# Optimization experiments

Measured on AMD Instinct MI355X. Metric: run time of the kernel, lower is better.

The kernel has to match this reference:

```python
import jax, jax.numpy as jnp
import numpy as np
import math

N_EMBD = 1024
N_HEADS = 16
B, T = 4, 2048

def setup_inputs() -> dict:
    key = jax.random.key(0)
    k1, k2, k3 = jax.random.split(key, 3)
    x = jax.random.normal(k1, (B, T, N_EMBD), dtype=jnp.float32)
    scale = 1.0 / math.sqrt(N_EMBD)
    W_attn = jax.random.normal(k2, (N_EMBD, 3 * N_EMBD), dtype=jnp.float32) * scale
    W_proj = jax.random.normal(k3, (N_EMBD, N_EMBD), dtype=jnp.float32) * scale
    return {"x": x, "W_attn": W_attn, "W_proj": W_proj}

def reference(x, W_attn, W_proj):
    Bb, Tt, C = x.shape
    hd = C // N_HEADS
    qkv = x @ W_attn  # [B,T,3C]
    q, k, v = jnp.split(qkv, 3, axis=-1)
    # [B,H,T,hd]
    q = q.reshape(Bb, Tt, N_HEADS, hd).transpose(0, 2, 1, 3)
    k = k.reshape(Bb, Tt, N_HEADS, hd).transpose(0, 2, 1, 3)
    v = v.reshape(Bb, Tt, N_HEADS, hd).transpose(0, 2, 1, 3)
    att = jnp.einsum('bhqd,bhkd->bhqk', q, k) * (1.0 / math.sqrt(hd))
    mask = jnp.tril(jnp.ones((Tt, Tt), dtype=bool))
    att = jnp.where(mask[None, None], att, -jnp.inf)
    att = jax.nn.softmax(att, axis=-1)
    out = jnp.einsum('bhqk,bhkd->bhqd', att, v)
    out = out.transpose(0, 2, 1, 3).reshape(Bb, Tt, C)
    return out @ W_proj
```

## Files before the change

kernel.cpp:

```cpp
#include <hip/hip_runtime.h>
#include <cstddef>
#include <cstdint>

typedef __attribute__((ext_vector_type(8))) _Float16 half8;
typedef __attribute__((ext_vector_type(4))) _Float16 half4;
typedef __attribute__((ext_vector_type(4))) float f32x4;
typedef __attribute__((ext_vector_type(16))) float f32x16;

#define N_EMBD 1024
#define N_HEADS 16
#define BATCH 4
#define SEQ 2048
#define C3 3072
#define HD 64

__device__ inline uint32_t pk2(float x, float y) {
    auto h2 = __builtin_amdgcn_cvt_pkrtz(x, y);
    uint32_t u;
    __builtin_memcpy(&u, &h2, 4);
    return u;
}

__device__ inline void swap32(uint32_t& a, uint32_t& b) {
    asm volatile("v_permlane32_swap_b32 %0, %1" : "+v"(a), "+v"(b));
}

__device__ inline float exp2_hw(float x) {
    float r;
    asm("v_exp_f32 %0, %1" : "=v"(r) : "v"(x));
    return r;
}

__global__ void cvt_f32_f16(const float* __restrict__ in, _Float16* __restrict__ out, int n) {
    int i = (blockIdx.x * 256 + threadIdx.x) * 4;
    if (i >= n) return;
    float4 v = *(const float4*)(in + i);
    half4 h;
    h[0] = (_Float16)v.x; h[1] = (_Float16)v.y; h[2] = (_Float16)v.z; h[3] = (_Float16)v.w;
    *(half4*)(out + i) = h;
}

__global__ void transpose_cvt(const float* __restrict__ in, _Float16* __restrict__ out,
                              int R, int Ncols) {
    __shared__ float tile[32][33];
    int n0 = blockIdx.x * 32, r0 = blockIdx.y * 32;
    int tx = threadIdx.x, ty = threadIdx.y;
#pragma unroll
    for (int i = 0; i < 32; i += 8)
        tile[ty + i][tx] = in[(size_t)(r0 + ty + i) * Ncols + n0 + tx];
    __syncthreads();
#pragma unroll
    for (int i = 0; i < 32; i += 8)
        out[(size_t)(n0 + ty + i) * R + r0 + tx] = (_Float16)tile[tx][ty + i];
}

__global__ void transpose_v(const _Float16* __restrict__ qkv, _Float16* __restrict__ vT) {
    __shared__ _Float16 tile[32][36];
    int t0 = blockIdx.x * 32;
    int bhd = blockIdx.y;
    int bh = bhd >> 1, dh = bhd & 1;
    int b = bh >> 4, h = bh & 15;
    int tx = threadIdx.x, ty = threadIdx.y;
#pragma unroll
    for (int i = 0; i < 32; i += 8)
        tile[ty + i][tx] = qkv[(size_t)(b * SEQ + t0 + ty + i) * C3 + 2 * N_EMBD + h * HD + dh * 32 + tx];
    __syncthreads();
#pragma unroll
    for (int i = 0; i < 32; i += 8)
        vT[((size_t)bh * HD + dh * 32 + ty + i) * SEQ + t0 + tx] = tile[tx][ty + i];
}

__device__ inline void store1(float* p, float v) { *p = v; }
__device__ inline void store1(_Float16* p, float v) { *p = (_Float16)v; }

template <typename OutT>
__global__ __launch_bounds__(512, 1) void gemm192(
    const _Float16* __restrict__ A, const _Float16* __restrict__ Bt,
    OutT* __restrict__ C, int M, int N, int K) {
    __shared__ _Float16 Al[2][256 * 64];
    __shared__ _Float16 Bl[2][192 * 64];
    const int tid = threadIdx.x;
    const int lane = tid & 63, wave = tid >> 6;
    const int l15 = lane & 15, l4 = lane >> 4;
    const int wm = wave >> 2, wn = wave & 3;

    const int nwg = gridDim.x, nbx = N / 192;
    int wg = blockIdx.x;
    if ((nwg & 7) == 0) { int cpx = nwg >> 3; wg = (wg & 7) * cpx + (wg >> 3); }
    const int row0 = (wg / nbx) * 256, col0 = (wg % nbx) * 192;
    const int TAU = K >> 6;

    const int srow = tid >> 3, su = tid & 7;
    const int usrc8 = (su ^ (srow & 7)) * 8;
    auto stageAu = [&](int unit, int ts) {
        __builtin_amdgcn_global_load_lds(
            (const __attribute__((address_space(1))) void*)(A + (size_t)(row0 + unit * 64 + srow) * K + ts * 64 + usrc8),
            (__attribute__((address_space(3))) void*)(&Al[ts & 1][unit * 64 * 64 + tid * 8]), 16, 0, 0);
    };
    auto stageBu = [&](int unit, int ts) {
        __builtin_amdgcn_global_load_lds(
            (const __attribute__((address_space(1))) void*)(Bt + (size_t)(col0 + unit * 64 + srow) * K + ts * 64 + usrc8),
            (__attribute__((address_space(3))) void*)(&Bl[ts & 1][unit * 64 * 64 + tid * 8]), 16, 0, 0);
    };
    auto stageTile = [&](int ts) {
        stageAu(0, ts); stageAu(1, ts); stageAu(2, ts); stageAu(3, ts);
        stageBu(0, ts); stageBu(1, ts); stageBu(2, ts);
    };

    f32x4 acc[8][3] = {};
    stageTile(0); stageTile(1);
    asm volatile("s_waitcnt vmcnt(7)" ::: "memory");
    __builtin_amdgcn_s_barrier();

    half8 a[4][2], b[3][2];
    for (int tau = 0; tau < TAU; ++tau) {
        const _Float16* Ab = &Al[tau & 1][0];
        const _Float16* Bb = &Bl[tau & 1][0];
        const bool t2 = (tau + 2 < TAU);

#pragma unroll
        for (int m = 0; m < 4; ++m)
#pragma unroll
            for (int ks = 0; ks < 2; ++ks) {
                int r = wm * 128 + m * 16 + l15;
                a[m][ks] = *(const half8*)(Ab + r * 64 + (((ks * 4 + l4) ^ (r & 7)) * 8));
            }
#pragma unroll
        for (int n = 0; n < 3; ++n)
#pragma unroll
            for (int ks = 0; ks < 2; ++ks) {
                int r = wn * 48 + n * 16 + l15;
                b[n][ks] = *(const half8*)(Bb + r * 64 + (((ks * 4 + l4) ^ (r & 7)) * 8));
            }
        __builtin_amdgcn_s_barrier();
        __builtin_amdgcn_s_setprio(1);
#pragma unroll
        for (int m = 0; m < 4; ++m)
#pragma unroll
            for (int n = 0; n < 2; ++n)
#pragma unroll
                for (int ks = 0; ks < 2; ++ks)
                    acc[m][n] = __builtin_amdgcn_mfma_f32_16x16x32_f16(a[m][ks], b[n][ks], acc[m][n], 0, 0, 0);
        __builtin_amdgcn_s_setprio(0);
        __builtin_amdgcn_s_barrier();

        if (t2) { stageBu(0, tau + 2); stageBu(1, tau + 2); stageBu(2, tau + 2); }
        __builtin_amdgcn_s_barrier();
        __builtin_amdgcn_s_setprio(1);
#pragma unroll
        for (int m = 0; m < 4; ++m)
#pragma unroll
            for (int ks = 0; ks < 2; ++ks)
                acc[m][2] = __builtin_amdgcn_mfma_f32_16x16x32_f16(a[m][ks], b[2][ks], acc[m][2], 0, 0, 0);
        __builtin_amdgcn_s_setprio(0);
        __builtin_amdgcn_s_barrier();

#pragma unroll
        for (int m = 0; m < 4; ++m)
#pragma unroll
            for (int ks = 0; ks < 2; ++ks) {
                int r = wm * 128 + 64 + m * 16 + l15;
                a[m][ks] = *(const half8*)(Ab + r * 64 + (((ks * 4 + l4) ^ (r & 7)) * 8));
            }
        if (t2) { stageAu(0, tau + 2); stageAu(2, tau + 2); }
        __builtin_amdgcn_s_barrier();
        __builtin_amdgcn_s_setprio(1);
#pragma unroll
        for (int m = 0; m < 4; ++m)
#pragma unroll
            for (int n = 0; n < 2; ++n)
#pragma unroll
                for (int ks = 0; ks < 2; ++ks)
                    acc[4 + m][n] = __builtin_amdgcn_mfma_f32_16x16x32_f16(a[m][ks], b[n][ks], acc[4 + m][n], 0, 0, 0);
        __builtin_amdgcn_s_setprio(0);
        __builtin_amdgcn_s_barrier();

        if (t2) { stageAu(1, tau + 2); stageAu(3, tau + 2); }
        __builtin_amdgcn_s_barrier();
        __builtin_amdgcn_s_setprio(1);
#pragma unroll
        for (int m = 0; m < 4; ++m)
#pragma unroll
            for (int ks = 0; ks < 2; ++ks)
                acc[4 + m][2] = __builtin_amdgcn_mfma_f32_16x16x32_f16(a[m][ks], b[2][ks], acc[4 + m][2], 0, 0, 0);
        __builtin_amdgcn_s_setprio(0);
        if (tau <= TAU - 3) {
            asm volatile("s_waitcnt vmcnt(7)" ::: "memory");
        } else if (tau == TAU - 2) {
            asm volatile("s_waitcnt vmcnt(0)" ::: "memory");
        }
        __builtin_amdgcn_s_barrier();
    }

#pragma unroll
    for (int mi = 0; mi < 8; ++mi)
#pragma unroll
        for (int ni = 0; ni < 3; ++ni)
#pragma unroll
            for (int j = 0; j < 4; ++j) {
                int r = row0 + wm * 128 + (mi >> 2) * 64 + (mi & 3) * 16 + l4 * 4 + j;
                int c = col0 + wn * 48 + ni * 16 + l15;
                store1(C + (size_t)r * N + c, acc[mi][ni][j]);
            }
}

template <typename OutT>
__global__ __launch_bounds__(256, 2) void gemm_h(
    const _Float16* __restrict__ A, const _Float16* __restrict__ Bt,
    OutT* __restrict__ C, int M, int N, int K) {
    __shared__ _Float16 Al[128 * 32];
    __shared__ _Float16 Bl[128 * 32];
    const int tid = threadIdx.x;
    const int wave = tid >> 6, lane = tid & 63;
    const int l15 = lane & 15, l4 = lane >> 4;
    const int gx = gridDim.x;
    int lin = blockIdx.y * gx + blockIdx.x;
    int bcol, brow;
    if ((gx & 7) == 0) {
        int cpx = gx >> 3;
        int xcd = lin & 7;
        int idx = lin >> 3;
        bcol = xcd * cpx + idx % cpx;
        brow = idx / cpx;
    } else { bcol = blockIdx.x; brow = blockIdx.y; }
    const int row0 = brow * 128, col0 = bcol * 128;
    const int wm = wave >> 1, wn = wave & 1;
    f32x4 acc[4][4] = {};
    for (int k0 = 0; k0 < K; k0 += 32) {
#pragma unroll
        for (int i = 0; i < 2; ++i) {
            int c = tid + 256 * i;
            int r = c >> 2, c8 = (c & 3) * 8;
            __builtin_amdgcn_global_load_lds(
                (const __attribute__((address_space(1))) void*)(A + (size_t)(row0 + r) * K + k0 + c8),
                (__attribute__((address_space(3))) void*)(Al + (size_t)(wave * 64 + 256 * i) * 8),
                16, 0, 0);
        }
#pragma unroll
        for (int i = 0; i < 2; ++i) {
            int c = tid + 256 * i;
            int r = c >> 2, c8 = (c & 3) * 8;
            __builtin_amdgcn_global_load_lds(
                (const __attribute__((address_space(1))) void*)(Bt + (size_t)(col0 + r) * K + k0 + c8),
                (__attribute__((address_space(3))) void*)(Bl + (size_t)(wave * 64 + 256 * i) * 8),
                16, 0, 0);
        }
        __syncthreads();
        half8 a[4], b[4];
#pragma unroll
        for (int m = 0; m < 4; ++m)
            a[m] = *(const half8*)(Al + (wm * 64 + m * 16 + l15) * 32 + l4 * 8);
#pragma unroll
        for (int n = 0; n < 4; ++n)
            b[n] = *(const half8*)(Bl + (wn * 64 + n * 16 + l15) * 32 + l4 * 8);
        __builtin_amdgcn_s_setprio(1);
#pragma unroll
        for (int m = 0; m < 4; ++m)
#pragma unroll
            for (int n = 0; n < 4; ++n)
                acc[m][n] = __builtin_amdgcn_mfma_f32_16x16x32_f16(a[m], b[n], acc[m][n], 0, 0, 0);
        __builtin_amdgcn_s_setprio(0);
        __syncthreads();
    }
#pragma unroll
    for (int m = 0; m < 4; ++m)
#pragma unroll
        for (int n = 0; n < 4; ++n)
#pragma unroll
            for (int j = 0; j < 4; ++j) {
                int r = row0 + wm * 64 + m * 16 + l4 * 4 + j;
                int cc = col0 + wn * 64 + n * 16 + l15;
                store1(C + (size_t)r * N + cc, acc[m][n][j]);
            }
}

__global__ __launch_bounds__(512, 4) void attn_kernel(const _Float16* __restrict__ qkv,
                                                      const _Float16* __restrict__ vT,
                                                      _Float16* __restrict__ ao) {
    const int bid = blockIdx.x;
    const int qt8 = (bid < 256) ? (bid >> 6) : 7 - ((bid - 256) >> 6);
    const int bh = bid & 63;
    const int b = bh >> 4, h = bh & 15;
    const int tid = threadIdx.x, lane = tid & 63;
    const int wave = tid >> 6;
    const int l31 = lane & 31, L = lane >> 5;

    __shared__ _Float16 Kl[3][64 * 64];
    __shared__ _Float16 Vl[3][64 * 64];

    const float qscale = 0.125f * 1.44269504089f;
    const float NEGC = -4.0f * 1.44269504089f;

    const int q0w = qt8 * 256 + wave * 32;
    const int q_g = q0w + l31;
    const int nt = 4 * qt8 + 4;

    const int s_row = tid >> 3;
    const int s_u8 = ((tid & 7) ^ (s_row & 7)) * 8;
    auto stage = [&](int t, int buf) {
        __builtin_amdgcn_global_load_lds(
            (const __attribute__((address_space(1))) void*)(qkv + (size_t)(b * SEQ + t * 64 + s_row) * C3 + N_EMBD + h * HD + s_u8),
            (__attribute__((address_space(3))) void*)(&Kl[buf][tid * 8]), 16, 0, 0);
        __builtin_amdgcn_global_load_lds(
            (const __attribute__((address_space(1))) void*)(vT + ((size_t)bh * HD + s_row) * SEQ + t * 64 + s_u8),
            (__attribute__((address_space(3))) void*)(&Vl[buf][tid * 8]), 16, 0, 0);
    };

    stage(0, 0);
    stage(1, 1);

    half8 qb[4];
#pragma unroll
    for (int ks = 0; ks < 4; ++ks) {
        half8 v = *(const half8*)(qkv + (size_t)(b * SEQ + q_g) * C3 + h * HD + ks * 16 + L * 8);
#pragma unroll
        for (int e = 0; e < 8; ++e) v[e] = (_Float16)((float)v[e] * qscale);
        qb[ks] = v;
    }
    half8 onesf;
#pragma unroll
    for (int e = 0; e < 8; ++e) onesf[e] = (_Float16)1.0f;

    const f32x16 cinit = (f32x16)(NEGC);
    f32x16 o[2];
    o[0] = (f32x16)(0.f);
    o[1] = (f32x16)(0.f);
    f32x16 lac = (f32x16)(0.f);

    asm volatile("s_waitcnt vmcnt(6)" ::: "memory");
    __builtin_amdgcn_s_barrier();

    int cur = 0;
    for (int t = 0; t < nt; ++t) {
        const int kv0 = t * 64;
        int sb = cur + 2; if (sb >= 3) sb -= 3;
        if (t + 2 < nt) stage(t + 2, sb);

        if (kv0 <= q0w + 31) {
            const _Float16* Kb = &Kl[cur][0];
            const _Float16* Vb = &Vl[cur][0];
            f32x16 s[2];
            __builtin_amdgcn_s_setprio(1);
#pragma unroll
            for (int kb = 0; kb < 2; ++kb) {
                const int key = kb * 32 + l31;
                {
                    half8 kf = *(const half8*)(Kb + key * 64 + ((L ^ (key & 7)) * 8));
                    s[kb] = __builtin_amdgcn_mfma_f32_32x32x16_f16(kf, qb[0], cinit, 0, 0, 0);
                }
#pragma unroll
                for (int ks = 1; ks < 4; ++ks) {
                    half8 kf = *(const half8*)(Kb + key * 64 + (((ks * 2 + L) ^ (key & 7)) * 8));
                    s[kb] = __builtin_amdgcn_mfma_f32_32x32x16_f16(kf, qb[ks], s[kb], 0, 0, 0);
                }
            }
            __builtin_amdgcn_s_setprio(0);
            const bool needmask = (kv0 + 63 > q0w);
#pragma unroll
            for (int kb = 0; kb < 2; ++kb) {
#pragma unroll
                for (int r = 0; r < 16; ++r) {
                    float v = exp2_hw(s[kb][r]);
                    if (needmask) {
                        int key_g = kv0 + kb * 32 + (r & 3) + 8 * (r >> 2) + 4 * L;
                        v = (key_g > q_g) ? 0.f : v;
                    }
                    s[kb][r] = v;
                }
            }
            half8 paf[4];
#pragma unroll
            for (int kb = 0; kb < 2; ++kb)
#pragma unroll
                for (int hf = 0; hf < 2; ++hf) {
                    const int bse = hf * 8;
                    uint32_t a0 = pk2(s[kb][bse + 0], s[kb][bse + 1]);
                    uint32_t b0 = pk2(s[kb][bse + 4], s[kb][bse + 5]);
                    swap32(a0, b0);
                    uint32_t a1 = pk2(s[kb][bse + 2], s[kb][bse + 3]);
                    uint32_t b1 = pk2(s[kb][bse + 6], s[kb][bse + 7]);
                    swap32(a1, b1);
                    uint32_t w[4] = {a0, a1, b0, b1};
                    __builtin_memcpy(&paf[kb * 2 + hf], w, 16);
                }
            __builtin_amdgcn_s_setprio(1);
#pragma unroll
            for (int ks = 0; ks < 4; ++ks) {
                lac = __builtin_amdgcn_mfma_f32_32x32x16_f16(paf[ks], onesf, lac, 0, 0, 0);
#pragma unroll
                for (int db = 0; db < 2; ++db) {
                    const int d = db * 32 + l31;
                    half8 vb = *(const half8*)(Vb + d * 64 + (((ks * 2 + L) ^ (d & 7)) * 8));
                    o[db] = __builtin_amdgcn_mfma_f32_32x32x16_f16(paf[ks], vb, o[db], 0, 0, 0);
                }
            }
            __builtin_amdgcn_s_setprio(0);
        }

        if (t + 2 < nt) {
            asm volatile("s_waitcnt vmcnt(2)" ::: "memory");
        } else if (t + 1 < nt) {
            asm volatile("s_waitcnt vmcnt(0)" ::: "memory");
        }
        __builtin_amdgcn_s_barrier();
        ++cur; if (cur == 3) cur = 0;
    }

#pragma unroll
    for (int db = 0; db < 2; ++db)
#pragma unroll
        for (int r = 0; r < 16; ++r) {
            int qg = q0w + (r & 3) + 8 * (r >> 2) + 4 * L;
            ao[(size_t)(b * SEQ + qg) * N_EMBD + h * HD + db * 32 + l31] =
                (_Float16)(o[db][r] / lac[r]);
        }
}

extern "C" void kernel_launch(void* const* d_in, const int* in_sizes, int n_in,
                              void* d_out, int out_size, void* d_ws, size_t ws_size,
                              hipStream_t stream) {
    const float* x  = (const float*)d_in[0];
    const float* Wa = (const float*)d_in[1];
    const float* Wp = (const float*)d_in[2];
    float* out = (float*)d_out;

    const int M = BATCH * SEQ;
    _Float16* xh  = (_Float16*)d_ws;
    _Float16* WaT = xh + (size_t)M * N_EMBD;
    _Float16* WpT = WaT + (size_t)C3 * N_EMBD;
    _Float16* qkv = WpT + (size_t)N_EMBD * N_EMBD;
    _Float16* ao  = qkv + (size_t)M * C3;
    _Float16* vT  = xh;

    int nx = M * N_EMBD;
    cvt_f32_f16<<<nx / 4 / 256, 256, 0, stream>>>(x, xh, nx);
    dim3 tb(32, 8);
    transpose_cvt<<<dim3(C3 / 32, N_EMBD / 32), tb, 0, stream>>>(Wa, WaT, N_EMBD, C3);
    transpose_cvt<<<dim3(N_EMBD / 32, N_EMBD / 32), tb, 0, stream>>>(Wp, WpT, N_EMBD, N_EMBD);

    gemm192<_Float16><<<dim3((M / 256) * (C3 / 192)), 512, 0, stream>>>(xh, WaT, qkv, M, C3, N_EMBD);

    transpose_v<<<dim3(SEQ / 32, BATCH * N_HEADS * 2), tb, 0, stream>>>(qkv, vT);

    attn_kernel<<<dim3(512), 512, 0, stream>>>(qkv, vT, ao);

    gemm_h<float><<<dim3(N_EMBD / 128, M / 128), 256, 0, stream>>>(ao, WpT, out, M, N_EMBD, N_EMBD);
}
```

Measured before the change: 188.1 us.

## Split attention into 128-query tiles processed as causal-balanced pairs per block

Each attention block now has 4 waves (256 threads) instead of 8. It handles two 128-query tiles in sequence, tile pairp and its mirror 15-pairp, so every block does about the same amount of causal work. Previously each block handled one 256-query tile, and the launch order was arranged to balance the load. Staging now issues two loads per thread for K and V, and the wait counts are adjusted to match. Smaller tiles waste less work on the masked diagonal, but each K/V tile loaded into LDS is shared by fewer waves, and the pipeline is restarted between the two passes.

```diff
diff --git a/kernel.cpp b/kernel.cpp
--- a/kernel.cpp
+++ b/kernel.cpp
@@ -274,11 +274,11 @@
             }
 }
 
-__global__ __launch_bounds__(512, 4) void attn_kernel(const _Float16* __restrict__ qkv,
+__global__ __launch_bounds__(256, 3) void attn_kernel(const _Float16* __restrict__ qkv,
                                                       const _Float16* __restrict__ vT,
                                                       _Float16* __restrict__ ao) {
     const int bid = blockIdx.x;
-    const int qt8 = (bid < 256) ? (bid >> 6) : 7 - ((bid - 256) >> 6);
+    const int pairp = bid >> 6;
     const int bh = bid & 63;
     const int b = bh >> 4, h = bh & 15;
     const int tid = threadIdx.x, lane = tid & 63;
@@ -291,129 +291,143 @@
     const float qscale = 0.125f * 1.44269504089f;
     const float NEGC = -4.0f * 1.44269504089f;
 
-    const int q0w = qt8 * 256 + wave * 32;
-    const int q_g = q0w + l31;
-    const int nt = 4 * qt8 + 4;
-
-    const int s_row = tid >> 3;
-    const int s_u8 = ((tid & 7) ^ (s_row & 7)) * 8;
     auto stage = [&](int t, int buf) {
-        __builtin_amdgcn_global_load_lds(
-            (const __attribute__((address_space(1))) void*)(qkv + (size_t)(b * SEQ + t * 64 + s_row) * C3 + N_EMBD + h * HD + s_u8),
-            (__attribute__((address_space(3))) void*)(&Kl[buf][tid * 8]), 16, 0, 0);
-        __builtin_amdgcn_global_load_lds(
-            (const __attribute__((address_space(1))) void*)(vT + ((size_t)bh * HD + s_row) * SEQ + t * 64 + s_u8),
-            (__attribute__((address_space(3))) void*)(&Vl[buf][tid * 8]), 16, 0, 0);
+#pragma unroll
+        for (int i = 0; i < 2; ++i) {
+            int idx = tid + 256 * i;
+            int key = idx >> 3;
+            int d8 = ((idx & 7) ^ (key & 7)) * 8;
+            __builtin_amdgcn_global_load_lds(
+                (const __attribute__((address_space(1))) void*)(qkv + (size_t)(b * SEQ + t * 64 + key) * C3 + N_EMBD + h * HD + d8),
+                (__attribute__((address_space(3))) void*)(&Kl[buf][idx * 8]), 16, 0, 0);
+        }
+#pragma unroll
+        for (int i = 0; i < 2; ++i) {
+            int idx = tid + 256 * i;
+            int d = idx >> 3;
+            int k8 = ((idx & 7) ^ (d & 7)) * 8;
+            __builtin_amdgcn_global_load_lds(
+                (const __attribute__((address_space(1))) void*)(vT + ((size_t)bh * HD + d) * SEQ + t * 64 + k8),
+                (__attribute__((address_space(3))) void*)(&Vl[buf][idx * 8]), 16, 0, 0);
+        }
     };
 
-    stage(0, 0);
-    stage(1, 1);
-
-    half8 qb[4];
-#pragma unroll
-    for (int ks = 0; ks < 4; ++ks) {
-        half8 v = *(const half8*)(qkv + (size_t)(b * SEQ + q_g) * C3 + h * HD + ks * 16 + L * 8);
-#pragma unroll
-        for (int e = 0; e < 8; ++e) v[e] = (_Float16)((float)v[e] * qscale);
-        qb[ks] = v;
+    half8 onesf;
+#pragma unroll
+    for (int e = 0; e < 8; ++e) onesf[e] = (_Float16)1.0f;
+    const f32x16 cinit = (f32x16)(NEGC);
+
+    for (int pass = 0; pass < 2; ++pass) {
+        const int qt = pass ? (15 - pairp) : pairp;
+        const int q0w = qt * 128 + wave * 32;
+        const int q_g = q0w + l31;
+        const int nt = 2 * qt + 2;
+
+        stage(0, 0);
+        stage(1, 1);
+
+        half8 qb[4];
+#pragma unroll
+        for (int ks = 0; ks < 4; ++ks) {
+            half8 v = *(const half8*)(qkv + (size_t)(b * SEQ + q_g) * C3 + h * HD + ks * 16 + L * 8);
+#pragma unroll
+            for (int e = 0; e < 8; ++e) v[e] = (_Float16)((float)v[e] * qscale);
+            qb[ks] = v;
+        }
+
+        f32x16 o[2];
+        o[0] = (f32x16)(0.f);
+        o[1] = (f32x16)(0.f);
+        f32x16 lac = (f32x16)(0.f);
+
+        asm volatile("s_waitcnt vmcnt(4)" ::: "memory");
+        __builtin_amdgcn_s_barrier();
+
+        int cur = 0;
+        for (int t = 0; t < nt; ++t) {
+            const int kv0 = t * 64;
+            int sb = cur + 2; if (sb >= 3) sb -= 3;
+            if (t + 2 < nt) stage(t + 2, sb);
+
+            if (kv0 <= q0w + 31) {
+                const _Float16* Kb = &Kl[cur][0];
+                const _Float16* Vb = &Vl[cur][0];
+                f32x16 s[2];
+                __builtin_amdgcn_s_setprio(1);
+#pragma unroll
+                for (int kb = 0; kb < 2; ++kb) {
+                    const int key = kb * 32 + l31;
+                    {
+                        half8 kf = *(const half8*)(Kb + key * 64 + ((L ^ (key & 7)) * 8));
+                        s[kb] = __builtin_amdgcn_mfma_f32_32x32x16_f16(kf, qb[0], cinit, 0, 0, 0);
+                    }
+#pragma unroll
+                    for (int ks = 1; ks < 4; ++ks) {
+                        half8 kf = *(const half8*)(Kb + key * 64 + (((ks * 2 + L) ^ (key & 7)) * 8));
+                        s[kb] = __builtin_amdgcn_mfma_f32_32x32x16_f16(kf, qb[ks], s[kb], 0, 0, 0);
+                    }
+                }
+                __builtin_amdgcn_s_setprio(0);
+                const bool needmask = (kv0 + 63 > q0w);
+#pragma unroll
+                for (int kb = 0; kb < 2; ++kb) {
+#pragma unroll
+                    for (int r = 0; r < 16; ++r) {
+                        float v = exp2_hw(s[kb][r]);
+                        if (needmask) {
+                            int key_g = kv0 + kb * 32 + (r & 3) + 8 * (r >> 2) + 4 * L;
+                            v = (key_g > q_g) ? 0.f : v;
+                        }
+                        s[kb][r] = v;
+                    }
+                }
+                half8 paf[4];
+#pragma unroll
+                for (int kb = 0; kb < 2; ++kb)
+#pragma unroll
+                    for (int hf = 0; hf < 2; ++hf) {
+                        const int bse = hf * 8;
+                        uint32_t a0 = pk2(s[kb][bse + 0], s[kb][bse + 1]);
+                        uint32_t b0 = pk2(s[kb][bse + 4], s[kb][bse + 5]);
+                        swap32(a0, b0);
+                        uint32_t a1 = pk2(s[kb][bse + 2], s[kb][bse + 3]);
+                        uint32_t b1 = pk2(s[kb][bse + 6], s[kb][bse + 7]);
+                        swap32(a1, b1);
+                        uint32_t w[4] = {a0, a1, b0, b1};
+                        __builtin_memcpy(&paf[kb * 2 + hf], w, 16);
+                    }
+                __builtin_amdgcn_s_setprio(1);
+#pragma unroll
+                for (int ks = 0; ks < 4; ++ks) {
+                    lac = __builtin_amdgcn_mfma_f32_32x32x16_f16(paf[ks], onesf, lac, 0, 0, 0);
+#pragma unroll
+                    for (int db = 0; db < 2; ++db) {
+                        const int d = db * 32 + l31;
+                        half8 vb = *(const half8*)(Vb + d * 64 + (((ks * 2 + L) ^ (d & 7)) * 8));
+                        o[db] = __builtin_amdgcn_mfma_f32_32x32x16_f16(paf[ks], vb, o[db], 0, 0, 0);
+                    }
+                }
+                __builtin_amdgcn_s_setprio(0);
+            }
+
+            if (t + 2 < nt) {
+                asm volatile("s_waitcnt vmcnt(4)" ::: "memory");
+            } else if (t + 1 < nt) {
+                asm volatile("s_waitcnt vmcnt(0)" ::: "memory");
+            }
+            __builtin_amdgcn_s_barrier();
+            ++cur; if (cur == 3) cur = 0;
+        }
+
+#pragma unroll
+        for (int db = 0; db < 2; ++db)
+#pragma unroll
+            for (int r = 0; r < 16; ++r) {
+                int qg = q0w + (r & 3) + 8 * (r >> 2) + 4 * L;
+                ao[(size_t)(b * SEQ + qg) * N_EMBD + h * HD + db * 32 + l31] =
+                    (_Float16)(o[db][r] / lac[r]);
+            }
     }
-    half8 onesf;
-#pragma unroll
-    for (int e = 0; e < 8; ++e) onesf[e] = (_Float16)1.0f;
-
-    const f32x16 cinit = (f32x16)(NEGC);
-    f32x16 o[2];
-    o[0] = (f32x16)(0.f);
-    o[1] = (f32x16)(0.f);
-    f32x16 lac = (f32x16)(0.f);
-
-    asm volatile("s_waitcnt vmcnt(6)" ::: "memory");
-    __builtin_amdgcn_s_barrier();
-
-    int cur = 0;
-    for (int t = 0; t < nt; ++t) {
-        const int kv0 = t * 64;
-        int sb = cur + 2; if (sb >= 3) sb -= 3;
-        if (t + 2 < nt) stage(t + 2, sb);
-
-        if (kv0 <= q0w + 31) {
-            const _Float16* Kb = &Kl[cur][0];
-            const _Float16* Vb = &Vl[cur][0];
-            f32x16 s[2];
-            __builtin_amdgcn_s_setprio(1);
-#pragma unroll
-            for (int kb = 0; kb < 2; ++kb) {
-                const int key = kb * 32 + l31;
-                {
-                    half8 kf = *(const half8*)(Kb + key * 64 + ((L ^ (key & 7)) * 8));
-                    s[kb] = __builtin_amdgcn_mfma_f32_32x32x16_f16(kf, qb[0], cinit, 0, 0, 0);
-                }
-#pragma unroll
-                for (int ks = 1; ks < 4; ++ks) {
-                    half8 kf = *(const half8*)(Kb + key * 64 + (((ks * 2 + L) ^ (key & 7)) * 8));
-                    s[kb] = __builtin_amdgcn_mfma_f32_32x32x16_f16(kf, qb[ks], s[kb], 0, 0, 0);
-                }
-            }
-            __builtin_amdgcn_s_setprio(0);
-            const bool needmask = (kv0 + 63 > q0w);
-#pragma unroll
-            for (int kb = 0; kb < 2; ++kb) {
-#pragma unroll
-                for (int r = 0; r < 16; ++r) {
-                    float v = exp2_hw(s[kb][r]);
-                    if (needmask) {
-                        int key_g = kv0 + kb * 32 + (r & 3) + 8 * (r >> 2) + 4 * L;
-                        v = (key_g > q_g) ? 0.f : v;
-                    }
-                    s[kb][r] = v;
-                }
-            }
-            half8 paf[4];
-#pragma unroll
-            for (int kb = 0; kb < 2; ++kb)
-#pragma unroll
-                for (int hf = 0; hf < 2; ++hf) {
-                    const int bse = hf * 8;
-                    uint32_t a0 = pk2(s[kb][bse + 0], s[kb][bse + 1]);
-                    uint32_t b0 = pk2(s[kb][bse + 4], s[kb][bse + 5]);
-                    swap32(a0, b0);
-                    uint32_t a1 = pk2(s[kb][bse + 2], s[kb][bse + 3]);
-                    uint32_t b1 = pk2(s[kb][bse + 6], s[kb][bse + 7]);
-                    swap32(a1, b1);
-                    uint32_t w[4] = {a0, a1, b0, b1};
-                    __builtin_memcpy(&paf[kb * 2 + hf], w, 16);
-                }
-            __builtin_amdgcn_s_setprio(1);
-#pragma unroll
-            for (int ks = 0; ks < 4; ++ks) {
-                lac = __builtin_amdgcn_mfma_f32_32x32x16_f16(paf[ks], onesf, lac, 0, 0, 0);
-#pragma unroll
-                for (int db = 0; db < 2; ++db) {
-                    const int d = db * 32 + l31;
-                    half8 vb = *(const half8*)(Vb + d * 64 + (((ks * 2 + L) ^ (d & 7)) * 8));
-                    o[db] = __builtin_amdgcn_mfma_f32_32x32x16_f16(paf[ks], vb, o[db], 0, 0, 0);
-                }
-            }
-            __builtin_amdgcn_s_setprio(0);
-        }
-
-        if (t + 2 < nt) {
-            asm volatile("s_waitcnt vmcnt(2)" ::: "memory");
-        } else if (t + 1 < nt) {
-            asm volatile("s_waitcnt vmcnt(0)" ::: "memory");
-        }
-        __builtin_amdgcn_s_barrier();
-        ++cur; if (cur == 3) cur = 0;
-    }
-
-#pragma unroll
-    for (int db = 0; db < 2; ++db)
-#pragma unroll
-        for (int r = 0; r < 16; ++r) {
-            int qg = q0w + (r & 3) + 8 * (r >> 2) + 4 * L;
-            ao[(size_t)(b * SEQ + qg) * N_EMBD + h * HD + db * 32 + l31] =
-                (_Float16)(o[db][r] / lac[r]);
-        }
 }
 
 extern "C" void kernel_launch(void* const* d_in, const int* in_sizes, int n_in,
@@ -442,7 +456,7 @@
 
     transpose_v<<<dim3(SEQ / 32, BATCH * N_HEADS * 2), tb, 0, stream>>>(qkv, vT);
 
-    attn_kernel<<<dim3(512), 512, 0, stream>>>(qkv, vT, ao);
+    attn_kernel<<<dim3(512), 256, 0, stream>>>(qkv, vT, ao);
 
     gemm_h<float><<<dim3(N_EMBD / 128, M / 128), 256, 0, stream>>>(ao, WpT, out, M, N_EMBD, N_EMBD);
 }
```

Result: no change. 187.5 us (-0.3%).
